# Performance work log

Measured on AMD Instinct MI355X. Metric: run time of the kernel, lower is better.

The kernel has to match this reference:

```python
import jax, jax.numpy as jnp
import numpy as np

VOCAB, POS_V, NER_V, DEPREL_V = 50000, 50, 10, 40
EMB, POS_D, NER_D, MEM = 300, 30, 30, 200
NUM_LAYERS = 2


def setup_inputs() -> dict:
    key = jax.random.key(0)
    ks = jax.random.split(key, 12)
    B, L = 32, 100
    adj = jax.random.randint(ks[0], (B, L, L), 0, DEPREL_V)
    words = jax.random.randint(ks[1], (B, L), 0, VOCAB)
    pos = jax.random.randint(ks[2], (B, L), 0, POS_V)
    ner = jax.random.randint(ks[3], (B, L), 0, NER_V)
    s = 0.02
    emb = jax.random.normal(ks[4], (VOCAB, EMB), jnp.float32) * s
    pos_emb = jax.random.normal(ks[5], (POS_V, POS_D), jnp.float32) * s
    ner_emb = jax.random.normal(ks[6], (NER_V, NER_D), jnp.float32) * s
    deprel_emb = jax.random.normal(ks[7], (DEPREL_V, MEM), jnp.float32) * s
    deprel_emb = deprel_emb.at[0].set(0.0)  # padding_idx=0
    in_dim = EMB + POS_D + NER_D
    Wp = jax.random.normal(ks[8], (MEM, in_dim), jnp.float32) * s
    bp = jnp.zeros((MEM,), jnp.float32)
    W0 = jax.random.normal(ks[9], (MEM, MEM), jnp.float32) * s
    b0 = jnp.zeros((MEM,), jnp.float32)
    W1 = jax.random.normal(ks[10], (MEM, MEM), jnp.float32) * s
    b1 = jnp.zeros((MEM,), jnp.float32)
    return {"adj": adj, "words": words, "pos": pos, "ner": ner,
            "emb": emb, "pos_emb": pos_emb, "ner_emb": ner_emb,
            "deprel_emb": deprel_emb, "Wp": Wp, "bp": bp,
            "W0": W0, "b0": b0, "W1": W1, "b1": b1}


def reference(adj, words, pos, ner, emb, pos_emb, ner_emb, deprel_emb,
              Wp, bp, W0, b0, W1, b1):
    # embedding lookups + concat  -> [B, L, in_dim]
    embs = jnp.concatenate([emb[words], pos_emb[pos], ner_emb[ner]], axis=-1)
    # preprocessor linear (diagonal_deprel branch)  -> [B, L, D]
    x = embs @ Wp.T + bp
    # per-edge relation embedding gather  -> [B, L, L, D]
    deprel_adj = deprel_emb[adj]
    adj_m = (adj != 0).astype(jnp.float32)            # [B, L, L]
    denom = adj_m.sum(2)[..., None] + 1.0             # [B, L, 1]
    mask = ((adj_m.sum(2) + adj_m.sum(1)) == 0)[..., None]  # [B, L, 1]
    for W, b in ((W0, b0), (W1, b1)):
        # diagonal deprel aggregation: (deprel_adj * x[:,None]) summed over neighbors
        Ax = jnp.einsum('blmd,bmd->bld', deprel_adj, x)
        AxW = (Ax @ W.T + b) + (x @ W.T + b)
        x = jax.nn.relu(AxW / denom)
    return x, mask
```

## Files before the change

### kernel.cpp

```cpp
#include <hip/hip_runtime.h>
#include <hip/hip_bf16.h>

#define BB 32
#define LL 100
#define DD 200
#define KIN 360
#define NP 3200
#define RNUM 40
#define LT 13
#define NT 8

__device__ __forceinline__ void fma4(float4& a, const float4& w, float s) {
    a.x = fmaf(w.x, s, a.x);
    a.y = fmaf(w.y, s, a.y);
    a.z = fmaf(w.z, s, a.z);
    a.w = fmaf(w.w, s, a.w);
}
__device__ __forceinline__ unsigned bf16rn(float f) {
    unsigned u = __float_as_uint(f);
    return (u + 0x7fffu + ((u >> 16) & 1u)) >> 16;
}
__device__ __forceinline__ unsigned pk2(float a, float b) {
    return bf16rn(a) | (bf16rn(b) << 16);
}
__device__ __forceinline__ float lo16(unsigned u) { return __uint_as_float(u << 16); }
__device__ __forceinline__ float hi16(unsigned u) { return __uint_as_float(u & 0xffff0000u); }

__global__ __launch_bounds__(512) void wpt_kernel(const float* __restrict__ Wp,
                                                  float* __restrict__ WpT) {
    int t = blockIdx.x * 512 + threadIdx.x;
    if (t < 18000) {
        int k = t / 50, o = (t % 50) * 4;
        float4 v;
        v.x = Wp[(size_t)(o + 0) * KIN + k];
        v.y = Wp[(size_t)(o + 1) * KIN + k];
        v.z = Wp[(size_t)(o + 2) * KIN + k];
        v.w = Wp[(size_t)(o + 3) * KIN + k];
        ((float4*)WpT)[t] = v;
    }
}

__global__ __launch_bounds__(512, 4) void embed_prep_kernel(
        const int* __restrict__ words, const int* __restrict__ pos, const int* __restrict__ ner,
        const float* __restrict__ emb, const float* __restrict__ pose, const float* __restrict__ nere,
        const float* __restrict__ wpt, const float* __restrict__ bp,
        const int* __restrict__ adj, const float* __restrict__ dep,
        const float* __restrict__ W0, const float* __restrict__ W1,
        float* __restrict__ W0T, float* __restrict__ W1T,
        uint2* __restrict__ depp_g, unsigned* __restrict__ adjp_g,
        float* __restrict__ xA, float* __restrict__ invd, float* __restrict__ mask_out) {
    __shared__ alignas(16) char smem[40960];
    int bid = blockIdx.x, tid = threadIdx.x;

    if (bid >= 476) {
        int i = (bid - 476) * 512 + tid;
        if (i < 80000) {
            int4 a = ((const int4*)adj)[i];
            adjp_g[i] = (unsigned)a.x | ((unsigned)a.y << 8) |
                        ((unsigned)a.z << 16) | ((unsigned)a.w << 24);
        }
        return;
    }
    if (bid >= 472) {
        int i = (bid - 472) * 512 + tid;
        if (i < 2000) {
            float4 v = ((const float4*)dep)[i];
            depp_g[i] = make_uint2(pk2(v.x, v.y), pk2(v.z, v.w));
        }
        return;
    }
    if (bid >= 432) {
        int i = (bid - 432) * 512 + tid;
        if (i < 10000) {
            int k = i / 50, o = (i % 50) * 4;
            float4 v;
            v.x = W0[(size_t)(o + 0) * DD + k];
            v.y = W0[(size_t)(o + 1) * DD + k];
            v.z = W0[(size_t)(o + 2) * DD + k];
            v.w = W0[(size_t)(o + 3) * DD + k];
            ((float4*)W0T)[i] = v;
        } else if (i < 20000) {
            int q = i - 10000;
            int k = q / 50, o = (q % 50) * 4;
            float4 v;
            v.x = W1[(size_t)(o + 0) * DD + k];
            v.y = W1[(size_t)(o + 1) * DD + k];
            v.z = W1[(size_t)(o + 2) * DD + k];
            v.w = W1[(size_t)(o + 3) * DD + k];
            ((float4*)W1T)[q] = v;
        }
        return;
    }

    if (bid >= 400) {
        int bb = bid - 400;
        int* a_lds = (int*)smem;
        int* rcc = (int*)(smem + 40000);
        const int4* src = (const int4*)(adj + (size_t)bb * (LL * LL));
        for (int i = tid; i < 2500; i += 512) ((int4*)a_lds)[i] = src[i];
        __syncthreads();
        if (tid < 200) {
            int l = tid % 100;
            int c = 0;
            if (tid < 100) {
                #pragma unroll 4
                for (int m = 0; m < 100; ++m) c += (a_lds[l * 100 + m] != 0);
            } else {
                #pragma unroll 4
                for (int m = 0; m < 100; ++m) c += (a_lds[m * 100 + l] != 0);
            }
            rcc[tid] = c;
        }
        __syncthreads();
        if (tid < 100) {
            int rc = rcc[tid], cc = rcc[100 + tid];
            invd[bb * 100 + tid] = 1.0f / (float)(rc + 1);
            mask_out[bb * 100 + tid] = (rc + cc == 0) ? 1.0f : 0.0f;
        }
        return;
    }

    float* es = (float*)smem;
    float4* red = (float4*)(smem + 11520);
    int pbase = bid * 8;

    float2* es2 = (float2*)es;
    for (int idx = tid; idx < 8 * 180; idx += 512) {
        int p = idx / 180, j2 = idx % 180;
        int gp = pbase + p;
        float2 v;
        if (j2 < 150)      v = ((const float2*)emb)[(size_t)words[gp] * 150 + j2];
        else if (j2 < 165) v = ((const float2*)pose)[pos[gp] * 15 + (j2 - 150)];
        else               v = ((const float2*)nere)[ner[gp] * 15 + (j2 - 165)];
        es2[idx] = v;
    }
    __syncthreads();

    int lane = tid & 63, w = tid >> 6;
    bool act = lane < 50;
    int oq = act ? lane : 49;
    int kq0 = (w < 5) ? 12 * w : 60 + 10 * (w - 5);
    int npair = (w < 5) ? 6 : 5;
    int kqlast = kq0 + 2 * npair - 1;
    const float4* wt4 = (const float4*)wpt;
    const float4* es4 = (const float4*)es;

    float4 a[8];
    #pragma unroll
    for (int p = 0; p < 8; ++p) a[p] = make_float4(0.f, 0.f, 0.f, 0.f);

    float4 wc[8], wn[8];
    #pragma unroll
    for (int q = 0; q < 2; ++q)
        #pragma unroll
        for (int j = 0; j < 4; ++j)
            wc[q * 4 + j] = wt4[(size_t)(4 * (kq0 + q) + j) * 50 + oq];

    for (int pr = 0; pr < npair; ++pr) {
        int nb = kq0 + 2 * pr + 2;
        int nbA = nb <= kqlast ? nb : kq0;
        int nbB = nb + 1 <= kqlast ? nb + 1 : kq0;
        #pragma unroll
        for (int j = 0; j < 4; ++j) wn[j]     = wt4[(size_t)(4 * nbA + j) * 50 + oq];
        #pragma unroll
        for (int j = 0; j < 4; ++j) wn[4 + j] = wt4[(size_t)(4 * nbB + j) * 50 + oq];
        #pragma unroll
        for (int q = 0; q < 2; ++q) {
            int kq = kq0 + 2 * pr + q;
            #pragma unroll
            for (int p = 0; p < 8; ++p) {
                float4 s = es4[p * 90 + kq];
                fma4(a[p], wc[q * 4 + 0], s.x); fma4(a[p], wc[q * 4 + 1], s.y);
                fma4(a[p], wc[q * 4 + 2], s.z); fma4(a[p], wc[q * 4 + 3], s.w);
            }
        }
        #pragma unroll
        for (int j = 0; j < 8; ++j) wc[j] = wn[j];
    }

    if (w >= 4 && act) {
        #pragma unroll
        for (int p = 0; p < 8; ++p) red[(w - 4) * 400 + p * 50 + oq] = a[p];
    }
    __syncthreads();
    if (w < 4 && act) {
        #pragma unroll
        for (int p = 0; p < 8; ++p) {
            float4 r = red[w * 400 + p * 50 + oq];
            r.x += a[p].x; r.y += a[p].y; r.z += a[p].z; r.w += a[p].w;
            red[w * 400 + p * 50 + oq] = r;
        }
    }
    __syncthreads();
    for (int t = tid; t < 400; t += 512) {
        int oq2 = t % 50;
        float4 v = ((const float4*)bp)[oq2];
        #pragma unroll
        for (int s = 0; s < 4; ++s) {
            float4 r = red[s * 400 + t];
            v.x += r.x; v.y += r.y; v.z += r.z; v.w += r.w;
        }
        ((float4*)xA)[(size_t)(pbase + t / 50) * 50 + oq2] = v;
    }
}

__global__ __launch_bounds__(1024, 4) void layer_kernel(
        const float* __restrict__ x,
        const uint2* __restrict__ depp_g, const unsigned* __restrict__ adjp_g,
        const float* __restrict__ wt, const float* __restrict__ bias,
        const float* __restrict__ invd, float* __restrict__ out) {
    __shared__ alignas(16) char smem[58912];
    uint2* deps_b = (uint2*)smem;
    unsigned* adjp = (unsigned*)(smem + 16000);
    float4* Sh = (float4*)(smem + 17312);
    float4* Sfin = (float4*)smem;

    int b = blockIdx.y, tile = blockIdx.x;
    int l0 = tile * LT;
    int lcnt = min(LT, LL - l0);
    int tid = threadIdx.x;
    const float4* x4 = (const float4*)x;

    for (int i = tid; i < 2000; i += 1024) deps_b[i] = depp_g[i];
    for (int i = tid; i < lcnt * 25; i += 1024)
        adjp[i] = adjp_g[(b * LL + l0) * 25 + i];
    __syncthreads();

    int lane = tid & 63, w = tid >> 6;
    int lg = w & 3, sq = w >> 2;
    bool act = lane < 50;
    int dq = lane;

    float4 acc[4];
    #pragma unroll
    for (int i = 0; i < 4; ++i) acc[i] = make_float4(0.f, 0.f, 0.f, 0.f);
    if (act) {
        int mg0 = (sq == 0) ? 0 : 1 + 6 * sq;
        int mg1 = mg0 + ((sq == 0) ? 7 : 6);
        float4 xc[4], xn[4];
        #pragma unroll
        for (int mm = 0; mm < 4; ++mm)
            xc[mm] = x4[(size_t)(b * LL + 4 * mg0 + mm) * 50 + dq];
        for (int mg = mg0; mg < mg1; ++mg) {
            int mgn = (mg + 1 < mg1) ? mg + 1 : mg;
            #pragma unroll
            for (int mm = 0; mm < 4; ++mm)
                xn[mm] = x4[(size_t)(b * LL + 4 * mgn + mm) * 50 + dq];
            unsigned ap[4];
            #pragma unroll
            for (int i = 0; i < 4; ++i) {
                int li = lg + 4 * i;
                ap[i] = (li < lcnt) ? adjp[li * 25 + mg] : 0u;
            }
            #pragma unroll
            for (int mm = 0; mm < 4; ++mm) {
                #pragma unroll
                for (int i = 0; i < 4; ++i) {
                    unsigned r = (ap[i] >> (8 * mm)) & 0xffu;
                    uint2 dv = deps_b[r * 50 + dq];
                    acc[i].x = fmaf(lo16(dv.x), xc[mm].x, acc[i].x);
                    acc[i].y = fmaf(hi16(dv.x), xc[mm].y, acc[i].y);
                    acc[i].z = fmaf(lo16(dv.y), xc[mm].z, acc[i].z);
                    acc[i].w = fmaf(hi16(dv.y), xc[mm].w, acc[i].w);
                }
            }
            #pragma unroll
            for (int mm = 0; mm < 4; ++mm) xc[mm] = xn[mm];
        }
        #pragma unroll
        for (int i = 0; i < 4; ++i) {
            int li = lg + 4 * i;
            if (li < lcnt) Sh[sq * 650 + li * 50 + dq] = acc[i];
        }
    }
    __syncthreads();

    for (int t2 = tid; t2 < 650; t2 += 1024) {
        int li = t2 / 50;
        if (li < lcnt) {
            float4 s0 = Sh[t2], s1 = Sh[650 + t2], s2 = Sh[1300 + t2], s3 = Sh[1950 + t2];
            float4 xr = x4[(size_t)(b * LL + l0 + li) * 50 + (t2 % 50)];
            float4 s;
            s.x = s0.x + s1.x + s2.x + s3.x + xr.x;
            s.y = s0.y + s1.y + s2.y + s3.y + xr.y;
            s.z = s0.z + s1.z + s2.z + s3.z + xr.z;
            s.w = s0.w + s1.w + s2.w + s3.w + xr.w;
            Sfin[t2] = s;
        }
    }
    __syncthreads();

    const float4* wt4 = (const float4*)wt;
    int oq = act ? lane : 49;
    int kq0 = (sq < 2) ? 13 * sq : 26 + 12 * (sq - 2);
    int kcnt = (sq < 2) ? 13 : 12;
    int npair = kcnt >> 1;
    int kqlast = kq0 + kcnt - 1;
    float4 ba[4];
    #pragma unroll
    for (int i = 0; i < 4; ++i) ba[i] = make_float4(0.f, 0.f, 0.f, 0.f);

    float4 wc[8], wn[8];
    #pragma unroll
    for (int q = 0; q < 2; ++q)
        #pragma unroll
        for (int j = 0; j < 4; ++j)
            wc[q * 4 + j] = wt4[(size_t)(4 * (kq0 + q) + j) * 50 + oq];

    int lic[4];
    #pragma unroll
    for (int i = 0; i < 4; ++i) {
        int li = lg + 4 * i;
        lic[i] = li < lcnt ? li : lcnt - 1;
    }

    for (int pr = 0; pr < npair; ++pr) {
        int nb = kq0 + 2 * pr + 2;
        int nbA = nb <= kqlast ? nb : kq0;
        int nbB = nb + 1 <= kqlast ? nb + 1 : kq0;
        #pragma unroll
        for (int j = 0; j < 4; ++j) wn[j]     = wt4[(size_t)(4 * nbA + j) * 50 + oq];
        #pragma unroll
        for (int j = 0; j < 4; ++j) wn[4 + j] = wt4[(size_t)(4 * nbB + j) * 50 + oq];
        #pragma unroll
        for (int q = 0; q < 2; ++q) {
            int kq = kq0 + 2 * pr + q;
            #pragma unroll
            for (int i = 0; i < 4; ++i) {
                float4 s = Sfin[lic[i] * 50 + kq];
                fma4(ba[i], wc[q * 4 + 0], s.x); fma4(ba[i], wc[q * 4 + 1], s.y);
                fma4(ba[i], wc[q * 4 + 2], s.z); fma4(ba[i], wc[q * 4 + 3], s.w);
            }
        }
        #pragma unroll
        for (int j = 0; j < 8; ++j) wc[j] = wn[j];
    }
    if (kcnt & 1) {
        #pragma unroll
        for (int i = 0; i < 4; ++i) {
            float4 s = Sfin[lic[i] * 50 + kqlast];
            fma4(ba[i], wc[0], s.x); fma4(ba[i], wc[1], s.y);
            fma4(ba[i], wc[2], s.z); fma4(ba[i], wc[3], s.w);
        }
    }

    if (act) {
        #pragma unroll
        for (int i = 0; i < 4; ++i) {
            int li = lg + 4 * i;
            if (li < lcnt) Sh[sq * 650 + li * 50 + oq] = ba[i];
        }
    }
    __syncthreads();

    for (int t2 = tid; t2 < 650; t2 += 1024) {
        int li = t2 / 50, oq2 = t2 % 50;
        if (li < lcnt) {
            float4 v0 = Sh[t2], v1 = Sh[650 + t2], v2 = Sh[1300 + t2], v3 = Sh[1950 + t2];
            float4 bb = ((const float4*)bias)[oq2];
            int p = b * LL + l0 + li;
            float sc = invd[p];
            float4 v;
            v.x = fmaxf((v0.x + v1.x + v2.x + v3.x + 2.f * bb.x) * sc, 0.f);
            v.y = fmaxf((v0.y + v1.y + v2.y + v3.y + 2.f * bb.y) * sc, 0.f);
            v.z = fmaxf((v0.z + v1.z + v2.z + v3.z + 2.f * bb.z) * sc, 0.f);
            v.w = fmaxf((v0.w + v1.w + v2.w + v3.w + 2.f * bb.w) * sc, 0.f);
            ((float4*)out)[(size_t)p * 50 + oq2] = v;
        }
    }
}

extern "C" void kernel_launch(void* const* d_in, const int* in_sizes, int n_in,
                              void* d_out, int out_size, void* d_ws, size_t ws_size,
                              hipStream_t stream) {
    const int*   adj   = (const int*)d_in[0];
    const int*   words = (const int*)d_in[1];
    const int*   pos   = (const int*)d_in[2];
    const int*   ner   = (const int*)d_in[3];
    const float* emb   = (const float*)d_in[4];
    const float* pose  = (const float*)d_in[5];
    const float* nere  = (const float*)d_in[6];
    const float* dep   = (const float*)d_in[7];
    const float* Wp    = (const float*)d_in[8];
    const float* bp    = (const float*)d_in[9];
    const float* W0    = (const float*)d_in[10];
    const float* b0    = (const float*)d_in[11];
    const float* W1    = (const float*)d_in[12];
    const float* b1    = (const float*)d_in[13];
    float* out = (float*)d_out;
    float* ws  = (float*)d_ws;

    float*    xA     = ws;
    float*    xB     = ws + 640000;
    float*    WpT    = ws + 1280000;
    float*    W0T    = ws + 1352000;
    float*    W1T    = ws + 1392000;
    float*    invd   = ws + 1432000;
    uint2*    depp_g = (uint2*)(ws + 1435200);
    unsigned* adjp_g = (unsigned*)(ws + 1439200);

    wpt_kernel<<<36, 512, 0, stream>>>(Wp, WpT);
    embed_prep_kernel<<<633, 512, 0, stream>>>(words, pos, ner, emb, pose, nere,
                                               WpT, bp, adj, dep, W0, W1, W0T, W1T,
                                               depp_g, adjp_g,
                                               xA, invd, out + (size_t)NP * DD);
    layer_kernel<<<dim3(NT, BB), 1024, 0, stream>>>(xA, depp_g, adjp_g, W0T, b0, invd, xB);
    layer_kernel<<<dim3(NT, BB), 1024, 0, stream>>>(xB, depp_g, adjp_g, W1T, b1, invd, out);
}
```

Measured before the change: 61.83 us.

## Replicate transposed weights per block group and stage per-batch x in LDS

The transposed weight matrices (WpT, W0T, W1T) are now written as 8 replicated copies, and each consuming block reads the copy chosen by its block or tile index. This spreads weight reads across different memory/L2 channels and cache lines to reduce contention. The layer kernel also loads the whole per-batch x slice (5000 float4) into LDS once, so both the aggregation loop and the residual read come from shared memory instead of global loads. In exchange, LDS use rises to about 139KB per block, which limits occupancy to one block per CU, and the prep kernels do 8x the transpose writes.

```diff
diff --git a/kernel.cpp b/kernel.cpp
--- a/kernel.cpp
+++ b/kernel.cpp
@@ -28,7 +28,8 @@
 
 __global__ __launch_bounds__(512) void wpt_kernel(const float* __restrict__ Wp,
                                                   float* __restrict__ WpT) {
-    int t = blockIdx.x * 512 + threadIdx.x;
+    int copy = blockIdx.x & 7;
+    int t = (blockIdx.x >> 3) * 512 + threadIdx.x;
     if (t < 18000) {
         int k = t / 50, o = (t % 50) * 4;
         float4 v;
@@ -36,7 +37,7 @@
         v.y = Wp[(size_t)(o + 1) * KIN + k];
         v.z = Wp[(size_t)(o + 2) * KIN + k];
         v.w = Wp[(size_t)(o + 3) * KIN + k];
-        ((float4*)WpT)[t] = v;
+        ((float4*)WpT)[(size_t)copy * 18000 + t] = v;
     }
 }
 
@@ -52,8 +53,8 @@
     __shared__ alignas(16) char smem[40960];
     int bid = blockIdx.x, tid = threadIdx.x;
 
-    if (bid >= 476) {
-        int i = (bid - 476) * 512 + tid;
+    if (bid >= 756) {
+        int i = (bid - 756) * 512 + tid;
         if (i < 80000) {
             int4 a = ((const int4*)adj)[i];
             adjp_g[i] = (unsigned)a.x | ((unsigned)a.y << 8) |
@@ -61,8 +62,8 @@
         }
         return;
     }
-    if (bid >= 472) {
-        int i = (bid - 472) * 512 + tid;
+    if (bid >= 752) {
+        int i = (bid - 752) * 512 + tid;
         if (i < 2000) {
             float4 v = ((const float4*)dep)[i];
             depp_g[i] = make_uint2(pk2(v.x, v.y), pk2(v.z, v.w));
@@ -70,7 +71,9 @@
         return;
     }
     if (bid >= 432) {
-        int i = (bid - 432) * 512 + tid;
+        int bid2 = bid - 432;
+        int copy = bid2 & 7;
+        int i = (bid2 >> 3) * 512 + tid;
         if (i < 10000) {
             int k = i / 50, o = (i % 50) * 4;
             float4 v;
@@ -78,7 +81,7 @@
             v.y = W0[(size_t)(o + 1) * DD + k];
             v.z = W0[(size_t)(o + 2) * DD + k];
             v.w = W0[(size_t)(o + 3) * DD + k];
-            ((float4*)W0T)[i] = v;
+            ((float4*)W0T)[(size_t)copy * 10000 + i] = v;
         } else if (i < 20000) {
             int q = i - 10000;
             int k = q / 50, o = (q % 50) * 4;
@@ -87,7 +90,7 @@
             v.y = W1[(size_t)(o + 1) * DD + k];
             v.z = W1[(size_t)(o + 2) * DD + k];
             v.w = W1[(size_t)(o + 3) * DD + k];
-            ((float4*)W1T)[q] = v;
+            ((float4*)W1T)[(size_t)copy * 10000 + q] = v;
         }
         return;
     }
@@ -142,7 +145,7 @@
     int kq0 = (w < 5) ? 12 * w : 60 + 10 * (w - 5);
     int npair = (w < 5) ? 6 : 5;
     int kqlast = kq0 + 2 * npair - 1;
-    const float4* wt4 = (const float4*)wpt;
+    const float4* wt4 = (const float4*)wpt + (size_t)(bid & 7) * 18000;
     const float4* es4 = (const float4*)es;
 
     float4 a[8];
@@ -209,18 +212,20 @@
         const uint2* __restrict__ depp_g, const unsigned* __restrict__ adjp_g,
         const float* __restrict__ wt, const float* __restrict__ bias,
         const float* __restrict__ invd, float* __restrict__ out) {
-    __shared__ alignas(16) char smem[58912];
-    uint2* deps_b = (uint2*)smem;
-    unsigned* adjp = (unsigned*)(smem + 16000);
-    float4* Sh = (float4*)(smem + 17312);
-    float4* Sfin = (float4*)smem;
+    __shared__ alignas(16) char smem[138912];
+    float4* x_lds = (float4*)smem;
+    uint2* deps_b = (uint2*)(smem + 80000);
+    unsigned* adjp = (unsigned*)(smem + 96000);
+    float4* Sh = (float4*)(smem + 97312);
+    float4* Sfin = (float4*)(smem + 80000);
 
     int b = blockIdx.y, tile = blockIdx.x;
     int l0 = tile * LT;
     int lcnt = min(LT, LL - l0);
     int tid = threadIdx.x;
-    const float4* x4 = (const float4*)x;
-
+
+    const float4* xg = (const float4*)x + (size_t)b * 5000;
+    for (int i = tid; i < 5000; i += 1024) x_lds[i] = xg[i];
     for (int i = tid; i < 2000; i += 1024) deps_b[i] = depp_g[i];
     for (int i = tid; i < lcnt * 25; i += 1024)
         adjp[i] = adjp_g[(b * LL + l0) * 25 + i];
@@ -237,15 +242,7 @@
     if (act) {
         int mg0 = (sq == 0) ? 0 : 1 + 6 * sq;
         int mg1 = mg0 + ((sq == 0) ? 7 : 6);
-        float4 xc[4], xn[4];
-        #pragma unroll
-        for (int mm = 0; mm < 4; ++mm)
-            xc[mm] = x4[(size_t)(b * LL + 4 * mg0 + mm) * 50 + dq];
         for (int mg = mg0; mg < mg1; ++mg) {
-            int mgn = (mg + 1 < mg1) ? mg + 1 : mg;
-            #pragma unroll
-            for (int mm = 0; mm < 4; ++mm)
-                xn[mm] = x4[(size_t)(b * LL + 4 * mgn + mm) * 50 + dq];
             unsigned ap[4];
             #pragma unroll
             for (int i = 0; i < 4; ++i) {
@@ -254,18 +251,17 @@
             }
             #pragma unroll
             for (int mm = 0; mm < 4; ++mm) {
+                float4 xv = x_lds[(4 * mg + mm) * 50 + dq];
                 #pragma unroll
                 for (int i = 0; i < 4; ++i) {
                     unsigned r = (ap[i] >> (8 * mm)) & 0xffu;
                     uint2 dv = deps_b[r * 50 + dq];
-                    acc[i].x = fmaf(lo16(dv.x), xc[mm].x, acc[i].x);
-                    acc[i].y = fmaf(hi16(dv.x), xc[mm].y, acc[i].y);
-                    acc[i].z = fmaf(lo16(dv.y), xc[mm].z, acc[i].z);
-                    acc[i].w = fmaf(hi16(dv.y), xc[mm].w, acc[i].w);
+                    acc[i].x = fmaf(lo16(dv.x), xv.x, acc[i].x);
+                    acc[i].y = fmaf(hi16(dv.x), xv.y, acc[i].y);
+                    acc[i].z = fmaf(lo16(dv.y), xv.z, acc[i].z);
+                    acc[i].w = fmaf(hi16(dv.y), xv.w, acc[i].w);
                 }
             }
-            #pragma unroll
-            for (int mm = 0; mm < 4; ++mm) xc[mm] = xn[mm];
         }
         #pragma unroll
         for (int i = 0; i < 4; ++i) {
@@ -279,7 +275,7 @@
         int li = t2 / 50;
         if (li < lcnt) {
             float4 s0 = Sh[t2], s1 = Sh[650 + t2], s2 = Sh[1300 + t2], s3 = Sh[1950 + t2];
-            float4 xr = x4[(size_t)(b * LL + l0 + li) * 50 + (t2 % 50)];
+            float4 xr = x_lds[(l0 + li) * 50 + (t2 % 50)];
             float4 s;
             s.x = s0.x + s1.x + s2.x + s3.x + xr.x;
             s.y = s0.y + s1.y + s2.y + s3.y + xr.y;
@@ -290,7 +286,7 @@
     }
     __syncthreads();
 
-    const float4* wt4 = (const float4*)wt;
+    const float4* wt4 = (const float4*)wt + (size_t)(tile & 7) * 10000;
     int oq = act ? lane : 49;
     int kq0 = (sq < 2) ? 13 * sq : 26 + 12 * (sq - 2);
     int kcnt = (sq < 2) ? 13 : 12;
@@ -393,14 +389,14 @@
     float*    xA     = ws;
     float*    xB     = ws + 640000;
     float*    WpT    = ws + 1280000;
-    float*    W0T    = ws + 1352000;
-    float*    W1T    = ws + 1392000;
-    float*    invd   = ws + 1432000;
-    uint2*    depp_g = (uint2*)(ws + 1435200);
-    unsigned* adjp_g = (unsigned*)(ws + 1439200);
-
-    wpt_kernel<<<36, 512, 0, stream>>>(Wp, WpT);
-    embed_prep_kernel<<<633, 512, 0, stream>>>(words, pos, ner, emb, pose, nere,
+    float*    W0T    = ws + 1856000;
+    float*    W1T    = ws + 2176000;
+    float*    invd   = ws + 2496000;
+    uint2*    depp_g = (uint2*)(ws + 2499200);
+    unsigned* adjp_g = (unsigned*)(ws + 2503200);
+
+    wpt_kernel<<<288, 512, 0, stream>>>(Wp, WpT);
+    embed_prep_kernel<<<913, 512, 0, stream>>>(words, pos, ner, emb, pose, nere,
                                                WpT, bp, adj, dep, W0, W1, W0T, W1T,
                                                depp_g, adjp_g,
                                                xA, invd, out + (size_t)NP * DD);
```

New measurement: 64.79 us. 1.05x slower.
